# Kernel tuning notes

Hardware: AMD Instinct MI355X
Metric: run time of the kernel (lower is better)

The kernel has to match this reference:

```python
import jax, jax.numpy as jnp
import numpy as np

OUT_FEAT = 32  # output_feature; projected dim = OUT_FEAT**2 = 1024
D_K = OUT_FEAT ** 0.5  # NOTE: source divides by sqrt(output_feature), not sqrt(output_feature^2)


def setup_inputs() -> dict:
    key = jax.random.key(0)
    ks = jax.random.split(key, 7)
    N, D_in, D_proj = 4096, 1024, OUT_FEAT * OUT_FEAT
    s = 1.0 / np.sqrt(D_in)
    return {
        "x": jax.random.normal(ks[0], (N, D_in), jnp.float32),
        "Wq": jax.random.normal(ks[1], (D_in, D_proj), jnp.float32) * s,
        "bq": jax.random.normal(ks[2], (D_proj,), jnp.float32) * s,
        "Wk": jax.random.normal(ks[3], (D_in, D_proj), jnp.float32) * s,
        "bk": jax.random.normal(ks[4], (D_proj,), jnp.float32) * s,
        "Wv": jax.random.normal(ks[5], (D_in, D_proj), jnp.float32) * s,
        "bv": jax.random.normal(ks[6], (D_proj,), jnp.float32) * s,
    }


def reference(x, Wq, bq, Wk, bk, Wv, bv):
    # QKV projections: [N, D_proj]
    Q = x @ Wq + bq
    K = x @ Wk + bk
    V = x @ Wv + bv
    # scores: [N, N], scaled by sqrt(output_feature) per the source
    scores = (Q @ K.T) / D_K
    attn_weights = jax.nn.softmax(scores, axis=-1)
    attn_output = attn_weights @ V  # [N, D_proj]
    attn_output = attn_output.reshape(-1, OUT_FEAT, OUT_FEAT)  # mode='cov' reshape
    return attn_output, attn_weights
```

## Files before the change

### kernel.cpp

```cpp
#include <hip/hip_runtime.h>

typedef short short8 __attribute__((ext_vector_type(8)));
typedef float f32x4 __attribute__((ext_vector_type(4)));

constexpr int NROW  = 4096;
constexpr int DIN   = 1024;
constexpr int DPROJ = 1024;
constexpr float INV_DK = 0.17677669529663687f;

__device__ __forceinline__ unsigned short f2bf(float f) {
  union { float f; unsigned int u; } v; v.f = f;
  unsigned int r = v.u + 0x7FFFu + ((v.u >> 16) & 1u);
  return (unsigned short)(r >> 16);
}
__device__ __forceinline__ float bf2f(unsigned short h) {
  union { unsigned int u; float f; } v; v.u = ((unsigned int)h) << 16; return v.f;
}

template<int KB>
__device__ __forceinline__ void stage_tile(const unsigned short* __restrict__ g,
                                           long row0, long ldK, long k0,
                                           unsigned short* lds_tile, int w, int lane) {
  if constexpr (KB == 64) {
    const int rsub = lane >> 3;
    const int csw  = ((lane & 7) ^ (rsub & 7)) * 8;
#pragma unroll
    for (int it = 0; it < 4; ++it) {
      const int rowblk = w * 32 + it * 8;
      const unsigned short* src = g + (row0 + rowblk + rsub) * ldK + k0 + csw;
      unsigned short* dst = lds_tile + rowblk * 64;
      __builtin_amdgcn_global_load_lds(
          (const __attribute__((address_space(1))) unsigned int*)(const void*)src,
          (__attribute__((address_space(3))) unsigned int*)(void*)dst, 16, 0, 0);
    }
  } else {
    const int rsub = lane >> 2;
    const int csw  = ((lane & 3) ^ ((rsub >> 1) & 3)) * 8;
#pragma unroll
    for (int it = 0; it < 2; ++it) {
      const int rowblk = w * 32 + it * 16;
      const unsigned short* src = g + (row0 + rowblk + rsub) * ldK + k0 + csw;
      unsigned short* dst = lds_tile + rowblk * 32;
      __builtin_amdgcn_global_load_lds(
          (const __attribute__((address_space(1))) unsigned int*)(const void*)src,
          (__attribute__((address_space(3))) unsigned int*)(void*)dst, 16, 0, 0);
    }
  }
}

template<int SPLIT, int EPI, int KB>
__global__ __launch_bounds__(256, 2) void mfma_gemm(
    const unsigned short* __restrict__ Ah, const unsigned short* __restrict__ Al,
    const unsigned short* __restrict__ Bh, const unsigned short* __restrict__ Bl,
    const float* __restrict__ bias, float* __restrict__ Cf,
    unsigned short* __restrict__ Coh, unsigned short* __restrict__ Col,
    int M, int N, int K, float alpha)
{
  constexpr int NT = SPLIT ? 4 : 2;
  constexpr int TS = 128 * KB;
  __shared__ __align__(16) unsigned short lds[2][NT * TS];
  const int tid  = threadIdx.x;
  const int w    = tid >> 6, lane = tid & 63;
  const int wr   = w >> 1,   wc   = w & 1;
  const int lrow = lane & 15, lgrp = lane >> 4;
  const long bm = (long)blockIdx.y * 128, bn = (long)blockIdx.x * 128;

  f32x4 acc[4][4] = {};
  const int nsteps = K / KB;

  stage_tile<KB>(Ah, bm, K, 0, &lds[0][0 * TS], w, lane);
  stage_tile<KB>(Bh, bn, K, 0, &lds[0][1 * TS], w, lane);
  if constexpr (SPLIT) {
    stage_tile<KB>(Al, bm, K, 0, &lds[0][2 * TS], w, lane);
    stage_tile<KB>(Bl, bn, K, 0, &lds[0][3 * TS], w, lane);
  }

  int cur = 0;
  for (int t = 0; t < nsteps; ++t) {
    __syncthreads();
    if (t + 1 < nsteps) {
      const long k0 = (long)(t + 1) * KB;
      const int nb = cur ^ 1;
      stage_tile<KB>(Ah, bm, K, k0, &lds[nb][0 * TS], w, lane);
      stage_tile<KB>(Bh, bn, K, k0, &lds[nb][1 * TS], w, lane);
      if constexpr (SPLIT) {
        stage_tile<KB>(Al, bm, K, k0, &lds[nb][2 * TS], w, lane);
        stage_tile<KB>(Bl, bn, K, k0, &lds[nb][3 * TS], w, lane);
      }
    }
    const unsigned short* L = lds[cur];
#pragma unroll
    for (int s = 0; s < KB / 32; ++s) {
      short8 ah[4], bh[4], al[4], bl[4];
#pragma unroll
      for (int i = 0; i < 4; ++i) {
        const int ra  = wr * 64 + i * 16 + lrow;
        const int sga = (KB == 64) ? (ra & 7) : ((ra >> 1) & 3);
        const int offa = ra * KB + ((s * 4 + lgrp) ^ sga) * 8;
        ah[i] = *(const short8*)&L[0 * TS + offa];
        if constexpr (SPLIT) al[i] = *(const short8*)&L[2 * TS + offa];
        const int rb  = wc * 64 + i * 16 + lrow;
        const int sgb = (KB == 64) ? (rb & 7) : ((rb >> 1) & 3);
        const int offb = rb * KB + ((s * 4 + lgrp) ^ sgb) * 8;
        bh[i] = *(const short8*)&L[1 * TS + offb];
        if constexpr (SPLIT) bl[i] = *(const short8*)&L[3 * TS + offb];
      }
#pragma unroll
      for (int i = 0; i < 4; ++i)
#pragma unroll
        for (int j = 0; j < 4; ++j) {
          acc[i][j] = __builtin_amdgcn_mfma_f32_16x16x32_bf16(ah[i], bh[j], acc[i][j], 0, 0, 0);
          if constexpr (SPLIT) {
            acc[i][j] = __builtin_amdgcn_mfma_f32_16x16x32_bf16(ah[i], bl[j], acc[i][j], 0, 0, 0);
            acc[i][j] = __builtin_amdgcn_mfma_f32_16x16x32_bf16(al[i], bh[j], acc[i][j], 0, 0, 0);
          }
        }
    }
    cur ^= 1;
  }

#pragma unroll
  for (int i = 0; i < 4; ++i) {
    const long rbase = bm + wr * 64 + i * 16 + lgrp * 4;
#pragma unroll
    for (int j = 0; j < 4; ++j) {
      const long cg = bn + wc * 64 + j * 16 + lrow;
#pragma unroll
      for (int r = 0; r < 4; ++r) {
        const long rg = rbase + r;
        float v = acc[i][j][r];
        if constexpr (EPI == 0) {
          Cf[rg * N + cg] = alpha * v;
        } else if constexpr (EPI == 1) {
          v += bias[cg];
          unsigned short h = f2bf(v);
          Coh[rg * N + cg] = h;
          Col[rg * N + cg] = f2bf(v - bf2f(h));
        } else {
          v += bias[rg];
          Coh[rg * N + cg] = f2bf(v);
        }
      }
    }
  }
}

__device__ __forceinline__ void stage256(const unsigned short* __restrict__ g,
    long row0, long ldK, long k0, unsigned short* tile, int w, int lane, int rnd)
{
  const int row_in = rnd * 128 + w * 16 + (lane >> 2);
  const int csw = ((lane & 3) ^ ((row_in >> 1) & 3)) * 8;
  const unsigned short* src = g + (row0 + row_in) * ldK + k0 + csw;
  unsigned short* dst = tile + (rnd * 128 + w * 16) * 32;
  __builtin_amdgcn_global_load_lds(
      (const __attribute__((address_space(1))) unsigned int*)(const void*)src,
      (__attribute__((address_space(3))) unsigned int*)(void*)dst, 16, 0, 0);
}

__global__ __launch_bounds__(512, 2) void score_gemm256(
    const unsigned short* __restrict__ Ah, const unsigned short* __restrict__ Al,
    const unsigned short* __restrict__ Bh, const unsigned short* __restrict__ Bl,
    float* __restrict__ Cf, int M, int N, int K, float alpha)
{
  __shared__ __align__(16) unsigned short lds[2][4 * 8192];
  const int tid  = threadIdx.x;
  const int w    = tid >> 6, lane = tid & 63;
  const int wr   = w >> 2,   wc   = w & 3;
  const int lrow = lane & 15, lgrp = lane >> 4;
  const long bm = (long)blockIdx.y * 256, bn = (long)blockIdx.x * 256;

  f32x4 acc[8][4] = {};
  const int nsteps = K >> 5;

  {
    unsigned short* B0 = &lds[0][0];
#pragma unroll
    for (int r = 0; r < 2; ++r) {
      stage256(Ah, bm, K, 0, B0 + 0 * 8192, w, lane, r);
      stage256(Al, bm, K, 0, B0 + 1 * 8192, w, lane, r);
      stage256(Bh, bn, K, 0, B0 + 2 * 8192, w, lane, r);
      stage256(Bl, bn, K, 0, B0 + 3 * 8192, w, lane, r);
    }
  }
  asm volatile("s_waitcnt vmcnt(0)" ::: "memory");

  int cur = 0;
  for (int t = 0; t < nsteps; ++t) {
    const unsigned short* L = &lds[cur][0];
    unsigned short* Ln = &lds[cur ^ 1][0];
    const long kn = (long)(t + 1) << 5;
    const bool pf = (t + 1 < nsteps);
#pragma unroll
    for (int q = 0; q < 4; ++q) {
      __builtin_amdgcn_s_barrier();
      __builtin_amdgcn_sched_barrier(0);
      const int mh = q >> 1, nh = q & 1;
      short8 a_h[4], a_l[4], b_h[2], b_l[2];
#pragma unroll
      for (int i = 0; i < 4; ++i) {
        const int ra = wr * 128 + mh * 64 + i * 16 + lrow;
        const int offa = ra * 32 + ((lgrp ^ ((ra >> 1) & 3)) * 8);
        a_h[i] = *(const short8*)&L[0 * 8192 + offa];
        a_l[i] = *(const short8*)&L[1 * 8192 + offa];
      }
#pragma unroll
      for (int j = 0; j < 2; ++j) {
        const int rb = wc * 64 + nh * 32 + j * 16 + lrow;
        const int offb = rb * 32 + ((lgrp ^ ((rb >> 1) & 3)) * 8);
        b_h[j] = *(const short8*)&L[2 * 8192 + offb];
        b_l[j] = *(const short8*)&L[3 * 8192 + offb];
      }
      if (pf && q == 0) {
#pragma unroll
        for (int r = 0; r < 2; ++r) {
          stage256(Ah, bm, K, kn, Ln + 0 * 8192, w, lane, r);
          stage256(Bh, bn, K, kn, Ln + 2 * 8192, w, lane, r);
        }
      }
      if (pf && q == 1) {
#pragma unroll
        for (int r = 0; r < 2; ++r) {
          stage256(Al, bm, K, kn, Ln + 1 * 8192, w, lane, r);
          stage256(Bl, bn, K, kn, Ln + 3 * 8192, w, lane, r);
        }
      }
      __builtin_amdgcn_sched_barrier(0);
      __builtin_amdgcn_s_setprio(1);
#pragma unroll
      for (int i = 0; i < 4; ++i)
#pragma unroll
        for (int j = 0; j < 2; ++j) {
          const int ai = mh * 4 + i, aj = nh * 2 + j;
          acc[ai][aj] = __builtin_amdgcn_mfma_f32_16x16x32_bf16(a_h[i], b_h[j], acc[ai][aj], 0, 0, 0);
          acc[ai][aj] = __builtin_amdgcn_mfma_f32_16x16x32_bf16(a_h[i], b_l[j], acc[ai][aj], 0, 0, 0);
          acc[ai][aj] = __builtin_amdgcn_mfma_f32_16x16x32_bf16(a_l[i], b_h[j], acc[ai][aj], 0, 0, 0);
        }
      __builtin_amdgcn_s_setprio(0);
      if (q == 3) {
        asm volatile("s_waitcnt vmcnt(0)" ::: "memory");
        __builtin_amdgcn_sched_barrier(0);
      }
    }
    cur ^= 1;
  }

#pragma unroll
  for (int i = 0; i < 8; ++i) {
    const long rbase = bm + wr * 128 + i * 16 + lgrp * 4;
#pragma unroll
    for (int j = 0; j < 4; ++j) {
      const long cg = bn + wc * 64 + j * 16 + lrow;
#pragma unroll
      for (int r = 0; r < 4; ++r)
        Cf[(rbase + r) * (long)N + cg] = alpha * acc[i][j][r];
    }
  }
}

__global__ __launch_bounds__(256) void split_rows(const float* __restrict__ in,
    unsigned short* __restrict__ oh, unsigned short* __restrict__ ol, int n4)
{
  int idx = blockIdx.x * 256 + threadIdx.x;
  const int stride = gridDim.x * 256;
  for (; idx < n4; idx += stride) {
    float4 v = ((const float4*)in)[idx];
    ushort4 h, l;
    h.x = f2bf(v.x); l.x = f2bf(v.x - bf2f(h.x));
    h.y = f2bf(v.y); l.y = f2bf(v.y - bf2f(h.y));
    h.z = f2bf(v.z); l.z = f2bf(v.z - bf2f(h.z));
    h.w = f2bf(v.w); l.w = f2bf(v.w - bf2f(h.w));
    ((ushort4*)oh)[idx] = h;
    ((ushort4*)ol)[idx] = l;
  }
}

__global__ __launch_bounds__(256) void split_transpose(const float* __restrict__ W,
    unsigned short* __restrict__ oTh, unsigned short* __restrict__ oTl, int R, int C)
{
  __shared__ float t[64][65];
  const int rt = blockIdx.y * 64, ct = blockIdx.x * 64;
  const int r0 = threadIdx.x >> 4, c4 = (threadIdx.x & 15) * 4;
#pragma unroll
  for (int rr = 0; rr < 4; ++rr) {
    const int row = r0 + rr * 16;
    float4 v = *(const float4*)(W + (long)(rt + row) * C + ct + c4);
    t[row][c4 + 0] = v.x; t[row][c4 + 1] = v.y;
    t[row][c4 + 2] = v.z; t[row][c4 + 3] = v.w;
  }
  __syncthreads();
#pragma unroll
  for (int rr = 0; rr < 4; ++rr) {
    const int orow = r0 + rr * 16;
    float x0 = t[c4 + 0][orow], x1 = t[c4 + 1][orow];
    float x2 = t[c4 + 2][orow], x3 = t[c4 + 3][orow];
    ushort4 h, l;
    h.x = f2bf(x0); l.x = f2bf(x0 - bf2f(h.x));
    h.y = f2bf(x1); l.y = f2bf(x1 - bf2f(h.y));
    h.z = f2bf(x2); l.z = f2bf(x2 - bf2f(h.z));
    h.w = f2bf(x3); l.w = f2bf(x3 - bf2f(h.w));
    *(ushort4*)(oTh + (long)(ct + orow) * R + rt + c4) = h;
    *(ushort4*)(oTl + (long)(ct + orow) * R + rt + c4) = l;
  }
}

__global__ __launch_bounds__(256) void softmax_p(float* __restrict__ S,
                                                 unsigned short* __restrict__ P)
{
  const int tid = threadIdx.x;
  float* p = S + (size_t)blockIdx.x * 4096;
  unsigned short* pb = P + (size_t)blockIdx.x * 4096;
  float4 v[4];
  float mx = -3.402823466e38f;
#pragma unroll
  for (int i = 0; i < 4; ++i) {
    v[i] = *(const float4*)(p + 4 * (tid + i * 256));
    mx = fmaxf(mx, fmaxf(fmaxf(v[i].x, v[i].y), fmaxf(v[i].z, v[i].w)));
  }
#pragma unroll
  for (int off = 32; off >= 1; off >>= 1) mx = fmaxf(mx, __shfl_xor(mx, off));
  __shared__ float redm[4], reds[4];
  if ((tid & 63) == 0) redm[tid >> 6] = mx;
  __syncthreads();
  mx = fmaxf(fmaxf(redm[0], redm[1]), fmaxf(redm[2], redm[3]));

  float sum = 0.f;
#pragma unroll
  for (int i = 0; i < 4; ++i) {
    v[i].x = __expf(v[i].x - mx); v[i].y = __expf(v[i].y - mx);
    v[i].z = __expf(v[i].z - mx); v[i].w = __expf(v[i].w - mx);
    sum += (v[i].x + v[i].y) + (v[i].z + v[i].w);
  }
#pragma unroll
  for (int off = 32; off >= 1; off >>= 1) sum += __shfl_xor(sum, off);
  if ((tid & 63) == 0) reds[tid >> 6] = sum;
  __syncthreads();
  sum = (reds[0] + reds[1]) + (reds[2] + reds[3]);
  const float inv = 1.0f / sum;
#pragma unroll
  for (int i = 0; i < 4; ++i) {
    v[i].x *= inv; v[i].y *= inv; v[i].z *= inv; v[i].w *= inv;
    *(float4*)(p + 4 * (tid + i * 256)) = v[i];
    ushort4 h;
    h.x = f2bf(v[i].x); h.y = f2bf(v[i].y); h.z = f2bf(v[i].z); h.w = f2bf(v[i].w);
    *(ushort4*)(pb + 4 * (tid + i * 256)) = h;
  }
}

extern "C" void kernel_launch(void* const* d_in, const int* in_sizes, int n_in,
                              void* d_out, int out_size, void* d_ws, size_t ws_size,
                              hipStream_t stream)
{
  const float* x  = (const float*)d_in[0];
  const float* Wq = (const float*)d_in[1];
  const float* bq = (const float*)d_in[2];
  const float* Wk = (const float*)d_in[3];
  const float* bk = (const float*)d_in[4];
  const float* Wv = (const float*)d_in[5];
  const float* bv = (const float*)d_in[6];

  float* attn_out = (float*)d_out;
  float* attn_w   = attn_out + (size_t)NROW * DPROJ;

  constexpr size_t MB = 1ull << 20;
  char* sc = (char*)attn_w;
  unsigned short* xh   = (unsigned short*)(sc + 0 * MB);
  unsigned short* xl   = (unsigned short*)(sc + 8 * MB);
  unsigned short* WqTh = (unsigned short*)(sc + 16 * MB);
  unsigned short* WqTl = (unsigned short*)(sc + 18 * MB);
  unsigned short* WkTh = (unsigned short*)(sc + 20 * MB);
  unsigned short* WkTl = (unsigned short*)(sc + 22 * MB);
  unsigned short* WvTh = (unsigned short*)(sc + 24 * MB);
  unsigned short* WvTl = (unsigned short*)(sc + 26 * MB);
  char* wsb = (char*)d_ws;
  unsigned short* VT = (unsigned short*)(wsb + 0 * MB);
  unsigned short* Qh = (unsigned short*)(wsb + 8 * MB);
  unsigned short* Ql = (unsigned short*)(wsb + 16 * MB);
  unsigned short* Kh = (unsigned short*)(wsb + 24 * MB);
  unsigned short* Kl = (unsigned short*)(wsb + 32 * MB);
  unsigned short* P  = (unsigned short*)(wsb + 8 * MB);

  dim3 blk(256);

  split_rows<<<4096, blk, 0, stream>>>(x, xh, xl, NROW * DIN / 4);
  dim3 gtr(16, 16);
  split_transpose<<<gtr, blk, 0, stream>>>(Wq, WqTh, WqTl, DIN, DPROJ);
  split_transpose<<<gtr, blk, 0, stream>>>(Wk, WkTh, WkTl, DIN, DPROJ);
  split_transpose<<<gtr, blk, 0, stream>>>(Wv, WvTh, WvTl, DIN, DPROJ);

  mfma_gemm<0, 3, 64><<<dim3(NROW / 128, DPROJ / 128), blk, 0, stream>>>(
      WvTh, nullptr, xh, nullptr, bv, nullptr, VT, nullptr,
      DPROJ, NROW, DIN, 1.0f);

  mfma_gemm<1, 1, 32><<<dim3(DPROJ / 128, NROW / 128), blk, 0, stream>>>(
      xh, xl, WqTh, WqTl, bq, nullptr, Qh, Ql, NROW, DPROJ, DIN, 1.0f);
  mfma_gemm<1, 1, 32><<<dim3(DPROJ / 128, NROW / 128), blk, 0, stream>>>(
      xh, xl, WkTh, WkTl, bk, nullptr, Kh, Kl, NROW, DPROJ, DIN, 1.0f);

  score_gemm256<<<dim3(NROW / 256, NROW / 256), dim3(512), 0, stream>>>(
      Qh, Ql, Kh, Kl, attn_w, NROW, NROW, DPROJ, INV_DK);

  softmax_p<<<NROW, blk, 0, stream>>>(attn_w, P);

  mfma_gemm<0, 0, 64><<<dim3(DPROJ / 128, NROW / 128), blk, 0, stream>>>(
      P, nullptr, VT, nullptr, nullptr, attn_out, nullptr, nullptr,
      NROW, DPROJ, NROW, 1.0f);
}
```

Measured before the change: 267.1 us.

## Merge Q/K projections into one launch and use 128x64 tiles for V and PV GEMMs

The separate Q and K projection GEMMs are folded into a single 512-block kernel that picks weights and outputs from the block index. The V projection and the P@V GEMM move to a new 128x64-tile kernel with its own 64-wide B staging routine. The smaller tiles double the block count, which on a 256-CU class device gives better wave fill for the 1024-wide outputs. The cost is less register-level reuse per block and more redundant A-tile loads.

```diff
diff --git a/kernel.cpp b/kernel.cpp
--- a/kernel.cpp
+++ b/kernel.cpp
@@ -48,74 +48,84 @@
   }
 }
 
-template<int SPLIT, int EPI, int KB>
-__global__ __launch_bounds__(256, 2) void mfma_gemm(
-    const unsigned short* __restrict__ Ah, const unsigned short* __restrict__ Al,
-    const unsigned short* __restrict__ Bh, const unsigned short* __restrict__ Bl,
-    const float* __restrict__ bias, float* __restrict__ Cf,
-    unsigned short* __restrict__ Coh, unsigned short* __restrict__ Col,
-    int M, int N, int K, float alpha)
-{
-  constexpr int NT = SPLIT ? 4 : 2;
-  constexpr int TS = 128 * KB;
-  __shared__ __align__(16) unsigned short lds[2][NT * TS];
-  const int tid  = threadIdx.x;
-  const int w    = tid >> 6, lane = tid & 63;
-  const int wr   = w >> 1,   wc   = w & 1;
-  const int lrow = lane & 15, lgrp = lane >> 4;
-  const long bm = (long)blockIdx.y * 128, bn = (long)blockIdx.x * 128;
+__device__ __forceinline__ void stage_tile64r(const unsigned short* __restrict__ g,
+                                              long row0, long ldK, long k0,
+                                              unsigned short* lds_tile, int w, int lane) {
+  const int rsub = lane >> 3;
+  const int csw  = ((lane & 7) ^ (rsub & 7)) * 8;
+#pragma unroll
+  for (int it = 0; it < 2; ++it) {
+    const int rowblk = w * 16 + it * 8;
+    const unsigned short* src = g + (row0 + rowblk + rsub) * ldK + k0 + csw;
+    unsigned short* dst = lds_tile + rowblk * 64;
+    __builtin_amdgcn_global_load_lds(
+        (const __attribute__((address_space(1))) unsigned int*)(const void*)src,
+        (__attribute__((address_space(3))) unsigned int*)(void*)dst, 16, 0, 0);
+  }
+}
+
+__global__ __launch_bounds__(256, 2) void qk_proj(
+    const unsigned short* __restrict__ xh, const unsigned short* __restrict__ xl,
+    const unsigned short* __restrict__ WqTh, const unsigned short* __restrict__ WqTl,
+    const unsigned short* __restrict__ WkTh, const unsigned short* __restrict__ WkTl,
+    const float* __restrict__ bq, const float* __restrict__ bk,
+    unsigned short* __restrict__ Qh, unsigned short* __restrict__ Ql,
+    unsigned short* __restrict__ Kh, unsigned short* __restrict__ Kl)
+{
+  constexpr int K = 1024, N = 1024, TS = 128 * 32;
+  __shared__ __align__(16) unsigned short lds[2][4 * TS];
+  const int tid = threadIdx.x, w = tid >> 6, lane = tid & 63;
+  const int wr = w >> 1, wc = w & 1, lrow = lane & 15, lgrp = lane >> 4;
+  const int which = blockIdx.x >> 8;
+  const int b = blockIdx.x & 255;
+  const long bm = (long)(b >> 3) * 128;
+  const long bn = (long)(b & 7) * 128;
+  const unsigned short* Bh = which ? WkTh : WqTh;
+  const unsigned short* Bl = which ? WkTl : WqTl;
+  const float* bias = which ? bk : bq;
+  unsigned short* Oh = which ? Kh : Qh;
+  unsigned short* Ol = which ? Kl : Ql;
 
   f32x4 acc[4][4] = {};
-  const int nsteps = K / KB;
-
-  stage_tile<KB>(Ah, bm, K, 0, &lds[0][0 * TS], w, lane);
-  stage_tile<KB>(Bh, bn, K, 0, &lds[0][1 * TS], w, lane);
-  if constexpr (SPLIT) {
-    stage_tile<KB>(Al, bm, K, 0, &lds[0][2 * TS], w, lane);
-    stage_tile<KB>(Bl, bn, K, 0, &lds[0][3 * TS], w, lane);
-  }
+  const int nsteps = K >> 5;
+
+  stage_tile<32>(xh, bm, K, 0, &lds[0][0 * TS], w, lane);
+  stage_tile<32>(Bh, bn, K, 0, &lds[0][1 * TS], w, lane);
+  stage_tile<32>(xl, bm, K, 0, &lds[0][2 * TS], w, lane);
+  stage_tile<32>(Bl, bn, K, 0, &lds[0][3 * TS], w, lane);
 
   int cur = 0;
   for (int t = 0; t < nsteps; ++t) {
     __syncthreads();
     if (t + 1 < nsteps) {
-      const long k0 = (long)(t + 1) * KB;
+      const long k0 = (long)(t + 1) << 5;
       const int nb = cur ^ 1;
-      stage_tile<KB>(Ah, bm, K, k0, &lds[nb][0 * TS], w, lane);
-      stage_tile<KB>(Bh, bn, K, k0, &lds[nb][1 * TS], w, lane);
-      if constexpr (SPLIT) {
-        stage_tile<KB>(Al, bm, K, k0, &lds[nb][2 * TS], w, lane);
-        stage_tile<KB>(Bl, bn, K, k0, &lds[nb][3 * TS], w, lane);
-      }
+      stage_tile<32>(xh, bm, K, k0, &lds[nb][0 * TS], w, lane);
+      stage_tile<32>(Bh, bn, K, k0, &lds[nb][1 * TS], w, lane);
+      stage_tile<32>(xl, bm, K, k0, &lds[nb][2 * TS], w, lane);
+      stage_tile<32>(Bl, bn, K, k0, &lds[nb][3 * TS], w, lane);
     }
     const unsigned short* L = lds[cur];
-#pragma unroll
-    for (int s = 0; s < KB / 32; ++s) {
-      short8 ah[4], bh[4], al[4], bl[4];
-#pragma unroll
-      for (int i = 0; i < 4; ++i) {
-        const int ra  = wr * 64 + i * 16 + lrow;
-        const int sga = (KB == 64) ? (ra & 7) : ((ra >> 1) & 3);
-        const int offa = ra * KB + ((s * 4 + lgrp) ^ sga) * 8;
-        ah[i] = *(const short8*)&L[0 * TS + offa];
-        if constexpr (SPLIT) al[i] = *(const short8*)&L[2 * TS + offa];
-        const int rb  = wc * 64 + i * 16 + lrow;
-        const int sgb = (KB == 64) ? (rb & 7) : ((rb >> 1) & 3);
-        const int offb = rb * KB + ((s * 4 + lgrp) ^ sgb) * 8;
-        bh[i] = *(const short8*)&L[1 * TS + offb];
-        if constexpr (SPLIT) bl[i] = *(const short8*)&L[3 * TS + offb];
-      }
-#pragma unroll
-      for (int i = 0; i < 4; ++i)
-#pragma unroll
-        for (int j = 0; j < 4; ++j) {
-          acc[i][j] = __builtin_amdgcn_mfma_f32_16x16x32_bf16(ah[i], bh[j], acc[i][j], 0, 0, 0);
-          if constexpr (SPLIT) {
-            acc[i][j] = __builtin_amdgcn_mfma_f32_16x16x32_bf16(ah[i], bl[j], acc[i][j], 0, 0, 0);
-            acc[i][j] = __builtin_amdgcn_mfma_f32_16x16x32_bf16(al[i], bh[j], acc[i][j], 0, 0, 0);
-          }
-        }
-    }
+    short8 ah[4], bh[4], al[4], bl[4];
+#pragma unroll
+    for (int i = 0; i < 4; ++i) {
+      const int ra = wr * 64 + i * 16 + lrow;
+      const int offa = ra * 32 + ((lgrp ^ ((ra >> 1) & 3)) * 8);
+      ah[i] = *(const short8*)&L[0 * TS + offa];
+      al[i] = *(const short8*)&L[2 * TS + offa];
+      const int rb = wc * 64 + i * 16 + lrow;
+      const int offb = rb * 32 + ((lgrp ^ ((rb >> 1) & 3)) * 8);
+      bh[i] = *(const short8*)&L[1 * TS + offb];
+      bl[i] = *(const short8*)&L[3 * TS + offb];
+    }
+#pragma unroll
+    for (int i = 0; i < 4; ++i)
+#pragma unroll
+      for (int j = 0; j < 4; ++j) {
+        acc[i][j] = __builtin_amdgcn_mfma_f32_16x16x32_bf16(ah[i], bh[j], acc[i][j], 0, 0, 0);
+        acc[i][j] = __builtin_amdgcn_mfma_f32_16x16x32_bf16(ah[i], bl[j], acc[i][j], 0, 0, 0);
+        acc[i][j] = __builtin_amdgcn_mfma_f32_16x16x32_bf16(al[i], bh[j], acc[i][j], 0, 0, 0);
+      }
     cur ^= 1;
   }
 
@@ -128,17 +138,81 @@
 #pragma unroll
       for (int r = 0; r < 4; ++r) {
         const long rg = rbase + r;
-        float v = acc[i][j][r];
+        float v = acc[i][j][r] + bias[cg];
+        unsigned short h = f2bf(v);
+        Oh[rg * N + cg] = h;
+        Ol[rg * N + cg] = f2bf(v - bf2f(h));
+      }
+    }
+  }
+}
+
+template<int EPI>
+__global__ __launch_bounds__(256, 2) void gemm_n64(
+    const unsigned short* __restrict__ A, const unsigned short* __restrict__ B,
+    const float* __restrict__ bias, float* __restrict__ Cf,
+    unsigned short* __restrict__ Co, int M, int N, int K)
+{
+  constexpr int TSA = 128 * 64;
+  constexpr int TSB = 64 * 64;
+  __shared__ __align__(16) unsigned short lds[2][TSA + TSB];
+  const int tid = threadIdx.x, w = tid >> 6, lane = tid & 63;
+  const int wr = w >> 1, wc = w & 1, lrow = lane & 15, lgrp = lane >> 4;
+  const long bm = (long)blockIdx.y * 128, bn = (long)blockIdx.x * 64;
+
+  f32x4 acc[4][2] = {};
+  const int nsteps = K >> 6;
+
+  stage_tile<64>(A, bm, K, 0, &lds[0][0], w, lane);
+  stage_tile64r(B, bn, K, 0, &lds[0][TSA], w, lane);
+
+  int cur = 0;
+  for (int t = 0; t < nsteps; ++t) {
+    __syncthreads();
+    if (t + 1 < nsteps) {
+      const long k0 = (long)(t + 1) << 6;
+      const int nb = cur ^ 1;
+      stage_tile<64>(A, bm, K, k0, &lds[nb][0], w, lane);
+      stage_tile64r(B, bn, K, k0, &lds[nb][TSA], w, lane);
+    }
+    const unsigned short* L = lds[cur];
+#pragma unroll
+    for (int s = 0; s < 2; ++s) {
+      short8 a[4], bb[2];
+#pragma unroll
+      for (int i = 0; i < 4; ++i) {
+        const int ra = wr * 64 + i * 16 + lrow;
+        const int offa = ra * 64 + (((s * 4 + lgrp) ^ (ra & 7)) * 8);
+        a[i] = *(const short8*)&L[offa];
+      }
+#pragma unroll
+      for (int j = 0; j < 2; ++j) {
+        const int rb = wc * 32 + j * 16 + lrow;
+        const int offb = rb * 64 + (((s * 4 + lgrp) ^ (rb & 7)) * 8);
+        bb[j] = *(const short8*)&L[TSA + offb];
+      }
+#pragma unroll
+      for (int i = 0; i < 4; ++i)
+#pragma unroll
+        for (int j = 0; j < 2; ++j)
+          acc[i][j] = __builtin_amdgcn_mfma_f32_16x16x32_bf16(a[i], bb[j], acc[i][j], 0, 0, 0);
+    }
+    cur ^= 1;
+  }
+
+#pragma unroll
+  for (int i = 0; i < 4; ++i) {
+    const long rbase = bm + wr * 64 + i * 16 + lgrp * 4;
+#pragma unroll
+    for (int j = 0; j < 2; ++j) {
+      const long cg = bn + wc * 32 + j * 16 + lrow;
+#pragma unroll
+      for (int r = 0; r < 4; ++r) {
+        const long rg = rbase + r;
         if constexpr (EPI == 0) {
-          Cf[rg * N + cg] = alpha * v;
-        } else if constexpr (EPI == 1) {
-          v += bias[cg];
-          unsigned short h = f2bf(v);
-          Coh[rg * N + cg] = h;
-          Col[rg * N + cg] = f2bf(v - bf2f(h));
+          Cf[rg * (long)N + cg] = acc[i][j][r];
         } else {
-          v += bias[rg];
-          Coh[rg * N + cg] = f2bf(v);
+          Co[rg * (long)N + cg] = f2bf(acc[i][j][r] + bias[rg]);
         }
       }
     }
@@ -387,21 +461,17 @@
   split_transpose<<<gtr, blk, 0, stream>>>(Wk, WkTh, WkTl, DIN, DPROJ);
   split_transpose<<<gtr, blk, 0, stream>>>(Wv, WvTh, WvTl, DIN, DPROJ);
 
-  mfma_gemm<0, 3, 64><<<dim3(NROW / 128, DPROJ / 128), blk, 0, stream>>>(
-      WvTh, nullptr, xh, nullptr, bv, nullptr, VT, nullptr,
-      DPROJ, NROW, DIN, 1.0f);
-
-  mfma_gemm<1, 1, 32><<<dim3(DPROJ / 128, NROW / 128), blk, 0, stream>>>(
-      xh, xl, WqTh, WqTl, bq, nullptr, Qh, Ql, NROW, DPROJ, DIN, 1.0f);
-  mfma_gemm<1, 1, 32><<<dim3(DPROJ / 128, NROW / 128), blk, 0, stream>>>(
-      xh, xl, WkTh, WkTl, bk, nullptr, Kh, Kl, NROW, DPROJ, DIN, 1.0f);
+  gemm_n64<3><<<dim3(NROW / 64, DPROJ / 128), blk, 0, stream>>>(
+      WvTh, xh, bv, nullptr, VT, DPROJ, NROW, DIN);
+
+  qk_proj<<<512, blk, 0, stream>>>(xh, xl, WqTh, WqTl, WkTh, WkTl,
+                                   bq, bk, Qh, Ql, Kh, Kl);
 
   score_gemm256<<<dim3(NROW / 256, NROW / 256), dim3(512), 0, stream>>>(
       Qh, Ql, Kh, Kl, attn_w, NROW, NROW, DPROJ, INV_DK);
 
   softmax_p<<<NROW, blk, 0, stream>>>(attn_w, P);
 
-  mfma_gemm<0, 0, 64><<<dim3(DPROJ / 128, NROW / 128), blk, 0, stream>>>(
-      P, nullptr, VT, nullptr, nullptr, attn_out, nullptr, nullptr,
-      NROW, DPROJ, NROW, 1.0f);
-}
+  gemm_n64<0><<<dim3(DPROJ / 64, NROW / 128), blk, 0, stream>>>(
+      P, VT, nullptr, attn_out, nullptr, NROW, DPROJ, NROW);
+}
```

After: 238.4 us. 1.12x faster.
